# Kernel tuning notes

Hardware: AMD Instinct MI355X
Metric: run time of the kernel (lower is better)

The kernel has to match this reference:

```python
import jax, jax.numpy as jnp
import numpy as np

N = 50000
E = 1600000
IN_C = 512
HID = 64
OUT_C = 64
HEADS = 2
K = 2
NEG_SLOPE = 0.2


def setup_inputs() -> dict:
    key = jax.random.key(0)
    ks = jax.random.split(key, 9)
    x = jax.random.normal(ks[0], (N, IN_C), dtype=jnp.float32)
    edge_index = jax.random.randint(ks[1], (2, E), 0, N, dtype=jnp.int64)
    edge_attr = jax.random.uniform(ks[2], (E,), dtype=jnp.float32)
    # SGConv linear (glorot-ish init)
    W_sg = jax.random.normal(ks[3], (IN_C, HID), dtype=jnp.float32) / np.sqrt(IN_C)
    b_sg = jnp.zeros((HID,), dtype=jnp.float32)
    # GATConv: lin (no bias), attention vectors, output bias (concat=False -> size OUT_C)
    W_gat = jax.random.normal(ks[4], (HID, HEADS * OUT_C), dtype=jnp.float32) / np.sqrt(HID)
    att_src = jax.random.normal(ks[5], (HEADS, OUT_C), dtype=jnp.float32) / np.sqrt(OUT_C)
    att_dst = jax.random.normal(ks[6], (HEADS, OUT_C), dtype=jnp.float32) / np.sqrt(OUT_C)
    b_gat = jnp.zeros((OUT_C,), dtype=jnp.float32)
    return {"x": x, "edge_index": edge_index, "edge_attr": edge_attr,
            "W_sg": W_sg, "b_sg": b_sg, "W_gat": W_gat,
            "att_src": att_src, "att_dst": att_dst, "b_gat": b_gat}


def reference(x, edge_index, edge_attr, W_sg, b_sg, W_gat, att_src, att_dst, b_gat):
    n = x.shape[0]
    src, dst = edge_index[0], edge_index[1]
    # add self-loops (weight 1) once; reused by SGConv (gcn_norm) and GAT
    loop = jnp.arange(n, dtype=src.dtype)
    src2 = jnp.concatenate([src, loop])
    dst2 = jnp.concatenate([dst, loop])
    ew = jnp.concatenate([edge_attr, jnp.ones((n,), x.dtype)])

    # ---- SGConv: K hops of D^-1/2 A D^-1/2, then linear ----
    deg = jax.ops.segment_sum(ew, dst2, num_segments=n)
    dinv = jnp.where(deg > 0, jax.lax.rsqrt(deg), 0.0)
    norm = dinv[src2] * ew * dinv[dst2]  # [E+N]
    h = x
    for _ in range(K):
        h = jax.ops.segment_sum(norm[:, None] * h[src2], dst2, num_segments=n)
    h = h @ W_sg + b_sg  # [N, HID]

    # activation (SELU); dropout is identity in eval mode
    h = jax.nn.selu(h)

    # ---- GATConv (heads, concat=False -> mean over heads) ----
    g = (h @ W_gat).reshape(n, HEADS, OUT_C)  # [N, H, C]
    a_src = jnp.einsum('nhc,hc->nh', g, att_src)  # [N, H]
    a_dst = jnp.einsum('nhc,hc->nh', g, att_dst)
    e = jax.nn.leaky_relu(a_src[src2] + a_dst[dst2], NEG_SLOPE)  # [E+N, H]
    # per-destination softmax (numerically stable)
    emax = jax.ops.segment_max(e, dst2, num_segments=n)
    emax = jnp.where(jnp.isfinite(emax), emax, 0.0)
    ee = jnp.exp(e - emax[dst2])
    denom = jax.ops.segment_sum(ee, dst2, num_segments=n)
    alpha = ee / jnp.maximum(denom[dst2], 1e-16)  # [E+N, H]
    out = jax.ops.segment_sum(alpha[:, :, None] * g[src2], dst2, num_segments=n)  # [N, H, C]
    return out.mean(axis=1) + b_gat  # [N, OUT_C]
```

## Files before the change

### kernel.cpp

```cpp
#include <hip/hip_runtime.h>
#include <hip/hip_fp16.h>
#include <math.h>

#define N_NODES 50000
#define N_EDGES 1600000
#define IN_CH 512
#define HID 64
#define OUTC 64
#define NEG_SLOPE 0.2f
#define EA_SCALE 131072.0f
#define PCAP 128
#define SLOTS 96

typedef __attribute__((ext_vector_type(8))) short bf16x8;
typedef __attribute__((ext_vector_type(4))) float f32x4;

__device__ __forceinline__ unsigned bf16r(float f) {
    unsigned b = __float_as_uint(f);
    return (b + 0x7FFFu + ((b >> 16) & 1u)) >> 16;
}

__device__ __forceinline__ void gload16(const void* g, void* l) {
    __builtin_amdgcn_global_load_lds(
        (const __attribute__((address_space(1))) void*)g,
        (__attribute__((address_space(3))) void*)l, 16, 0, 0);
}

__global__ void k_wsplit(const float* __restrict__ W, short* __restrict__ Wfrag) {
    int idx = blockIdx.x * 256 + threadIdx.x;
    if (idx >= IN_CH * HID) return;
    int k = idx >> 6, c = idx & 63;
    float wv = W[idx];
    unsigned h = bf16r(wv);
    float res = wv - __uint_as_float(h << 16);
    unsigned l = bf16r(res);
    int kstep = k >> 5, cb = c >> 4;
    int lane = (c & 15) | (((k >> 3) & 3) << 4);
    int j = k & 7;
    int base = ((kstep * 4 + cb) * 2) * 512 + lane * 8 + j;
    Wfrag[base] = (short)h;
    Wfrag[base + 512] = (short)l;
}

#define G1R 64
#define G1KC 64
__global__ __launch_bounds__(256) void k_gemm_hist(const float* __restrict__ x,
                                                   const short* __restrict__ Wfrag,
                                                   __half* __restrict__ p,
                                                   const int* __restrict__ src,
                                                   const int* __restrict__ dst,
                                                   const float* __restrict__ ea,
                                                   unsigned* __restrict__ deg32,
                                                   int2* __restrict__ edges2) {
    __shared__ float xs[2][G1R][G1KC];
    int tid = threadIdx.x;
    int bid = blockIdx.x;

    if (bid & 1) {
        int e0 = (bid >> 1) * 2048;
        int e1 = e0 + 2048; if (e1 > N_EDGES) e1 = N_EDGES;
        for (int e = e0 + tid; e < e1; e += 256) {
            int d = dst[e];
            float w = ea[e];
            unsigned pack = (1u << 24) | (unsigned)(w * EA_SCALE);
            unsigned old = atomicAdd(&deg32[d], pack);
            int rank = (int)(old >> 24);
            edges2[d * SLOTS + rank] = make_int2(src[e] << 5, __float_as_int(w));
        }
        return;
    }

    int lane = tid & 63, wv = tid >> 6;
    int r0 = (bid >> 1) * G1R;
    f32x4 acc0 = {0.f, 0.f, 0.f, 0.f};
    f32x4 acc1 = {0.f, 0.f, 0.f, 0.f};
    f32x4 acc2 = {0.f, 0.f, 0.f, 0.f};
    f32x4 acc3 = {0.f, 0.f, 0.f, 0.f};

    auto stage = [&](int b, int k0) {
#pragma unroll
        for (int it = 0; it < 4; it++) {
            int rowbase = it * 16 + wv * 4;
            int row = rowbase + (lane >> 4);
            int gr = r0 + row; if (gr > N_NODES - 1) gr = N_NODES - 1;
            int col = ((lane & 15) ^ (row & 7)) << 2;
            gload16(x + (size_t)gr * IN_CH + k0 + col, &xs[b][rowbase][0]);
        }
    };

    stage(0, 0);
    asm volatile("s_waitcnt vmcnt(0)" ::: "memory");
    __syncthreads();

    int cur = 0;
    int arow = wv * 16 + (lane & 15);
    const char* xsbase = (const char*)&xs[0][0][0];
    for (int k0 = 0; k0 < IN_CH; k0 += G1KC) {
        if (k0 + G1KC < IN_CH) stage(cur ^ 1, k0 + G1KC);
#pragma unroll
        for (int kk = 0; kk < 2; kk++) {
            int ks = (k0 >> 5) + kk;
            const short* wb = Wfrag + ks * 4096 + (lane << 3);
            bf16x8 bh0 = *(const bf16x8*)(wb);
            bf16x8 bl0 = *(const bf16x8*)(wb + 512);
            bf16x8 bh1 = *(const bf16x8*)(wb + 1024);
            bf16x8 bl1 = *(const bf16x8*)(wb + 1536);
            bf16x8 bh2 = *(const bf16x8*)(wb + 2048);
            bf16x8 bl2 = *(const bf16x8*)(wb + 2560);
            bf16x8 bh3 = *(const bf16x8*)(wb + 3072);
            bf16x8 bl3 = *(const bf16x8*)(wb + 3584);
            int c16 = kk * 8 + ((lane >> 4) << 1);
            size_t rb = (size_t)cur * (G1R * G1KC * 4) + (size_t)arow * (G1KC * 4);
            float4 xa = *(const float4*)(xsbase + rb + (((c16    ) ^ (arow & 7)) << 4));
            float4 xb = *(const float4*)(xsbase + rb + (((c16 + 1) ^ (arow & 7)) << 4));
            float xv[8] = {xa.x, xa.y, xa.z, xa.w, xb.x, xb.y, xb.z, xb.w};
            bf16x8 ah, al;
#pragma unroll
            for (int j = 0; j < 8; j++) {
                unsigned b = __float_as_uint(xv[j]);
                float res = xv[j] - __uint_as_float(b & 0xFFFF0000u);
                ah[j] = (short)(b >> 16);
                al[j] = (short)(__float_as_uint(res) >> 16);
            }
            acc0 = __builtin_amdgcn_mfma_f32_16x16x32_bf16(ah, bh0, acc0, 0, 0, 0);
            acc0 = __builtin_amdgcn_mfma_f32_16x16x32_bf16(ah, bl0, acc0, 0, 0, 0);
            acc0 = __builtin_amdgcn_mfma_f32_16x16x32_bf16(al, bh0, acc0, 0, 0, 0);
            acc1 = __builtin_amdgcn_mfma_f32_16x16x32_bf16(ah, bh1, acc1, 0, 0, 0);
            acc1 = __builtin_amdgcn_mfma_f32_16x16x32_bf16(ah, bl1, acc1, 0, 0, 0);
            acc1 = __builtin_amdgcn_mfma_f32_16x16x32_bf16(al, bh1, acc1, 0, 0, 0);
            acc2 = __builtin_amdgcn_mfma_f32_16x16x32_bf16(ah, bh2, acc2, 0, 0, 0);
            acc2 = __builtin_amdgcn_mfma_f32_16x16x32_bf16(ah, bl2, acc2, 0, 0, 0);
            acc2 = __builtin_amdgcn_mfma_f32_16x16x32_bf16(al, bh2, acc2, 0, 0, 0);
            acc3 = __builtin_amdgcn_mfma_f32_16x16x32_bf16(ah, bh3, acc3, 0, 0, 0);
            acc3 = __builtin_amdgcn_mfma_f32_16x16x32_bf16(ah, bl3, acc3, 0, 0, 0);
            acc3 = __builtin_amdgcn_mfma_f32_16x16x32_bf16(al, bh3, acc3, 0, 0, 0);
        }
        asm volatile("s_waitcnt vmcnt(0)" ::: "memory");
        __syncthreads();
        cur ^= 1;
    }
    int crow = r0 + wv * 16 + ((lane >> 4) << 2);
    int ccol = lane & 15;
#pragma unroll
    for (int r = 0; r < 4; r++) {
        int gr = crow + r;
        if (gr < N_NODES) {
            p[(unsigned)gr * HID + ccol]      = __float2half(acc0[r]);
            p[(unsigned)gr * HID + 16 + ccol] = __float2half(acc1[r]);
            p[(unsigned)gr * HID + 32 + ccol] = __float2half(acc2[r]);
            p[(unsigned)gr * HID + 48 + ccol] = __float2half(acc3[r]);
        }
    }
}

__global__ void k_dinv(const unsigned* __restrict__ deg32, float* __restrict__ dinv) {
    int i = blockIdx.x * 256 + threadIdx.x;
    if (i < N_NODES)
        dinv[i] = rsqrtf(1.0f + (float)(deg32[i] & 0xFFFFFFu) * (1.0f / EA_SCALE));
}

__global__ void k_hscale(unsigned* __restrict__ h2, const float* __restrict__ dinv) {
    int idx = blockIdx.x * 256 + threadIdx.x;
    if (idx >= N_NODES * 32) return;
    float dv = dinv[idx >> 5];
    unsigned u = h2[idx];
    float2 f = __half22float2(*(__half2*)&u);
    __half2 r = __floats2half2_rn(f.x * dv, f.y * dv);
    h2[idx] = *(unsigned*)&r;
}

__global__ __launch_bounds__(256) void k_hop(const unsigned* __restrict__ hin2,
                                             const unsigned* __restrict__ deg32,
                                             const int2* __restrict__ edges2,
                                             const float* __restrict__ dinv,
                                             unsigned* __restrict__ hout2,
                                             int pw) {
    __shared__ float2 part[2][32];
    int tid = threadIdx.x;
    int w = tid >> 6, lane = tid & 63;
    int slot = w >> 1, half = w & 1;
    int cl = lane & 31, es = lane >> 5;
    int v = blockIdx.x * 2 + slot;
    int cnt = (int)(deg32[v] >> 24);
    int beg = v * SLOTS, end = beg + cnt;
    int mid = beg + (cnt >> 1);
    int lo = half ? mid : beg;
    int hi = half ? end : mid;
    float ax = 0.f, ay = 0.f, bx = 0.f, by = 0.f;
    float cx = 0.f, cy = 0.f, dx = 0.f, dy = 0.f;
    if (!half && !es) {
        unsigned gh = hin2[(unsigned)v * 32 + cl];
        float2 hf = __half22float2(*(__half2*)&gh);
        ax = hf.x; ay = hf.y;
    }
    int i = lo;
    for (; i + 16 <= hi; i += 16) {
        int2 e0 = edges2[i + es];
        int2 e1 = edges2[i + 2 + es];
        int2 e2 = edges2[i + 4 + es];
        int2 e3 = edges2[i + 6 + es];
        int2 e4 = edges2[i + 8 + es];
        int2 e5 = edges2[i + 10 + es];
        int2 e6 = edges2[i + 12 + es];
        int2 e7 = edges2[i + 14 + es];
        unsigned g0 = hin2[(unsigned)(e0.x + cl)];
        unsigned g1 = hin2[(unsigned)(e1.x + cl)];
        unsigned g2 = hin2[(unsigned)(e2.x + cl)];
        unsigned g3 = hin2[(unsigned)(e3.x + cl)];
        unsigned g4 = hin2[(unsigned)(e4.x + cl)];
        unsigned g5 = hin2[(unsigned)(e5.x + cl)];
        unsigned g6 = hin2[(unsigned)(e6.x + cl)];
        unsigned g7 = hin2[(unsigned)(e7.x + cl)];
        float w0 = __int_as_float(e0.y), w1 = __int_as_float(e1.y);
        float w2 = __int_as_float(e2.y), w3 = __int_as_float(e3.y);
        float w4 = __int_as_float(e4.y), w5 = __int_as_float(e5.y);
        float w6 = __int_as_float(e6.y), w7 = __int_as_float(e7.y);
        float2 h0 = __half22float2(*(__half2*)&g0);
        float2 h1 = __half22float2(*(__half2*)&g1);
        float2 h2 = __half22float2(*(__half2*)&g2);
        float2 h3 = __half22float2(*(__half2*)&g3);
        float2 h4 = __half22float2(*(__half2*)&g4);
        float2 h5 = __half22float2(*(__half2*)&g5);
        float2 h6 = __half22float2(*(__half2*)&g6);
        float2 h7 = __half22float2(*(__half2*)&g7);
        ax += w0 * h0.x; ay += w0 * h0.y;
        bx += w1 * h1.x; by += w1 * h1.y;
        cx += w2 * h2.x; cy += w2 * h2.y;
        dx += w3 * h3.x; dy += w3 * h3.y;
        ax += w4 * h4.x; ay += w4 * h4.y;
        bx += w5 * h5.x; by += w5 * h5.y;
        cx += w6 * h6.x; cy += w6 * h6.y;
        dx += w7 * h7.x; dy += w7 * h7.y;
    }
    for (; i + 8 <= hi; i += 8) {
        int2 e0 = edges2[i + es];
        int2 e1 = edges2[i + 2 + es];
        int2 e2 = edges2[i + 4 + es];
        int2 e3 = edges2[i + 6 + es];
        unsigned g0 = hin2[(unsigned)(e0.x + cl)];
        unsigned g1 = hin2[(unsigned)(e1.x + cl)];
        unsigned g2 = hin2[(unsigned)(e2.x + cl)];
        unsigned g3 = hin2[(unsigned)(e3.x + cl)];
        float w0 = __int_as_float(e0.y), w1 = __int_as_float(e1.y);
        float w2 = __int_as_float(e2.y), w3 = __int_as_float(e3.y);
        float2 h0 = __half22float2(*(__half2*)&g0);
        float2 h1 = __half22float2(*(__half2*)&g1);
        float2 h2 = __half22float2(*(__half2*)&g2);
        float2 h3 = __half22float2(*(__half2*)&g3);
        ax += w0 * h0.x; ay += w0 * h0.y;
        bx += w1 * h1.x; by += w1 * h1.y;
        cx += w2 * h2.x; cy += w2 * h2.y;
        dx += w3 * h3.x; dy += w3 * h3.y;
    }
    for (; i + es < hi; i += 2) {
        int2 e0 = edges2[i + es];
        unsigned g0 = hin2[(unsigned)(e0.x + cl)];
        float w0 = __int_as_float(e0.y);
        float2 h0 = __half22float2(*(__half2*)&g0);
        ax += w0 * h0.x; ay += w0 * h0.y;
    }
    ax += bx + cx + dx; ay += by + cy + dy;
    ax += __shfl_xor(ax, 32);
    ay += __shfl_xor(ay, 32);
    if (half && lane < 32) part[slot][cl] = make_float2(ax, ay);
    __syncthreads();
    if (!half && lane < 32) {
        float dv = dinv[v];
        float sc = (pw == 2) ? dv * dv : dv;
        float2 pp = part[slot][cl];
        __half2 hp = __floats2half2_rn(sc * (ax + pp.x), sc * (ay + pp.y));
        hout2[(unsigned)v * 32 + cl] = *(unsigned*)&hp;
    }
}

#define G2_ROWS 32
__global__ __launch_bounds__(256) void k_act_gemm2(const __half* __restrict__ h2,
                                                   const float* __restrict__ bsg,
                                                   const float* __restrict__ Wg,
                                                   const float* __restrict__ att_s,
                                                   const float* __restrict__ att_d,
                                                   uint2* __restrict__ g4h,
                                                   float2* __restrict__ asrc2,
                                                   float4* __restrict__ admm) {
    __shared__ float hs[G2_ROWS][HID];
    int tid = threadIdx.x;
    int wave = tid >> 6, lane = tid & 63;
    int r0 = blockIdx.x * G2_ROWS;
    int rbase = wave * 8;

    const float SC = 1.0507009873554805f, AL = 1.6732632423543772f;
    {
        int row = tid >> 3, c0 = (tid & 7) * 8;
        int r = r0 + row;
        float vals[8];
        if (r < N_NODES) {
            uint4 raw = *(const uint4*)(h2 + (unsigned)r * HID + c0);
            float2 f0 = __half22float2(*(__half2*)&raw.x);
            float2 f1 = __half22float2(*(__half2*)&raw.y);
            float2 f2 = __half22float2(*(__half2*)&raw.z);
            float2 f3 = __half22float2(*(__half2*)&raw.w);
            vals[0] = f0.x; vals[1] = f0.y; vals[2] = f1.x; vals[3] = f1.y;
            vals[4] = f2.x; vals[5] = f2.y; vals[6] = f3.x; vals[7] = f3.y;
        } else {
#pragma unroll
            for (int j = 0; j < 8; j++) vals[j] = 0.f;
        }
#pragma unroll
        for (int j = 0; j < 8; j++) {
            float hv = vals[j] + bsg[c0 + j];
            hv = (hv > 0.f) ? SC * hv : SC * AL * (__expf(hv) - 1.f);
            hs[row][c0 + j] = hv;
        }
    }
    __syncthreads();

    float accx[8], accy[8];
#pragma unroll
    for (int j = 0; j < 8; j++) { accx[j] = 0.f; accy[j] = 0.f; }
#pragma unroll 2
    for (int k = 0; k < HID; k++) {
        float w0 = Wg[(size_t)k * 128 + lane];
        float w1 = Wg[(size_t)k * 128 + 64 + lane];
#pragma unroll
        for (int j = 0; j < 8; j++) {
            float hk = hs[rbase + j][k];
            accx[j] += hk * w0;
            accy[j] += hk * w1;
        }
    }
    float ats0 = att_s[lane], ats1 = att_s[64 + lane];
    float atd0 = att_d[lane], atd1 = att_d[64 + lane];
#pragma unroll
    for (int j = 0; j < 8; j++) {
        int v = r0 + rbase + j;
        if (v >= N_NODES) break;
        __half2 gp = __floats2half2_rn(accx[j], accy[j]);
        unsigned gpu = *(unsigned*)&gp;
        unsigned other = (unsigned)__shfl_xor((int)gpu, 1);
        if (!(lane & 1)) g4h[(unsigned)v * 32 + (lane >> 1)] = make_uint2(gpu, other);
        float s0 = accx[j] * ats0, s1 = accy[j] * ats1;
        float d0 = accx[j] * atd0, d1 = accy[j] * atd1;
#pragma unroll
        for (int o = 32; o > 0; o >>= 1) {
            s0 += __shfl_xor(s0, o);
            s1 += __shfl_xor(s1, o);
            d0 += __shfl_xor(d0, o);
            d1 += __shfl_xor(d1, o);
        }
        if (lane == 0) {
            asrc2[v] = make_float2(s0, s1);
            float m0 = s0 + d0; m0 = (m0 > 0.f) ? m0 : NEG_SLOPE * m0;
            float m1 = s1 + d1; m1 = (m1 > 0.f) ? m1 : NEG_SLOPE * m1;
            admm[v] = make_float4(d0, d1, m0, m1);
        }
    }
}

__global__ __launch_bounds__(256) void k_gat(const uint2* __restrict__ g4h,
                                             const float2* __restrict__ asrc2,
                                             const float4* __restrict__ admm,
                                             const unsigned* __restrict__ deg32,
                                             const int2* __restrict__ edges2,
                                             const float* __restrict__ bgat,
                                             float* __restrict__ out) {
    __shared__ int4 pbuf[2][2][PCAP];
    __shared__ float4 pacc[2][32];
    __shared__ float2 pden[2][32];
    int tid = threadIdx.x;
    int w = tid >> 6, lane = tid & 63;
    int slot = w >> 1, half = w & 1;
    int cl = lane & 31, es = lane >> 5;
    int v = blockIdx.x * 2 + slot;
    float4 am = admm[v];
    int cnt = (int)(deg32[v] >> 24);
    int beg = v * SLOTS, end = beg + cnt;
    int mid = beg + (cnt >> 1);
    int lo = half ? mid : beg;
    int hi = half ? end : mid;
    int n = hi - lo;

    float pd0 = 0.f, pd1 = 0.f;
    for (int i = lo + lane; i < hi; i += 64) {
        int2 e = edges2[i];
        float2 a = asrc2[(unsigned)e.x >> 5];
        float t0 = a.x + am.x; t0 = (t0 > 0.f) ? t0 : NEG_SLOPE * t0;
        float t1 = a.y + am.y; t1 = (t1 > 0.f) ? t1 : NEG_SLOPE * t1;
        float p0 = __expf(t0 - am.z);
        float p1 = __expf(t1 - am.w);
        int idx = i - lo;
        if (idx < PCAP)
            pbuf[slot][half][idx] = make_int4(e.x, __float_as_int(p0), __float_as_int(p1), 0);
        pd0 += p0; pd1 += p1;
    }
#pragma unroll
    for (int o = 32; o > 0; o >>= 1) {
        pd0 += __shfl_xor(pd0, o);
        pd1 += __shfl_xor(pd1, o);
    }
    if (!half) { pd0 += 1.f; pd1 += 1.f; }

    float aA = 0.f, aB = 0.f, aC = 0.f, aD = 0.f;
    float bA = 0.f, bB = 0.f, bC = 0.f, bD = 0.f;
    if (!half && !es) {
        uint2 gs = g4h[(unsigned)v * 32 + cl];
        float2 gx = __half22float2(*(__half2*)&gs.x);
        float2 gy = __half22float2(*(__half2*)&gs.y);
        aA = gx.x; aB = gx.y; aC = gy.x; aD = gy.y;
    }
    int n1 = (n < PCAP) ? n : PCAP;
    int ii = 0;
    for (; ii + 8 <= n1; ii += 8) {
        int4 e0 = pbuf[slot][half][ii + es];
        int4 e1 = pbuf[slot][half][ii + 2 + es];
        int4 e2 = pbuf[slot][half][ii + 4 + es];
        int4 e3 = pbuf[slot][half][ii + 6 + es];
        uint2 g0 = g4h[(unsigned)(e0.x + cl)];
        uint2 g1 = g4h[(unsigned)(e1.x + cl)];
        uint2 g2 = g4h[(unsigned)(e2.x + cl)];
        uint2 g3 = g4h[(unsigned)(e3.x + cl)];
        float p00 = __int_as_float(e0.y), p01 = __int_as_float(e0.z);
        float p10 = __int_as_float(e1.y), p11 = __int_as_float(e1.z);
        float p20 = __int_as_float(e2.y), p21 = __int_as_float(e2.z);
        float p30 = __int_as_float(e3.y), p31 = __int_as_float(e3.z);
        float2 g0x = __half22float2(*(__half2*)&g0.x);
        float2 g0y = __half22float2(*(__half2*)&g0.y);
        float2 g1x = __half22float2(*(__half2*)&g1.x);
        float2 g1y = __half22float2(*(__half2*)&g1.y);
        float2 g2x = __half22float2(*(__half2*)&g2.x);
        float2 g2y = __half22float2(*(__half2*)&g2.y);
        float2 g3x = __half22float2(*(__half2*)&g3.x);
        float2 g3y = __half22float2(*(__half2*)&g3.y);
        aA += p00 * g0x.x; aB += p01 * g0x.y; aC += p00 * g0y.x; aD += p01 * g0y.y;
        bA += p10 * g1x.x; bB += p11 * g1x.y; bC += p10 * g1y.x; bD += p11 * g1y.y;
        aA += p20 * g2x.x; aB += p21 * g2x.y; aC += p20 * g2y.x; aD += p21 * g2y.y;
        bA += p30 * g3x.x; bB += p31 * g3x.y; bC += p30 * g3y.x; bD += p31 * g3y.y;
    }
    for (; ii + es < n1; ii += 2) {
        int4 e0 = pbuf[slot][half][ii + es];
        uint2 g0 = g4h[(unsigned)(e0.x + cl)];
        float p00 = __int_as_float(e0.y), p01 = __int_as_float(e0.z);
        float2 g0x = __half22float2(*(__half2*)&g0.x);
        float2 g0y = __half22float2(*(__half2*)&g0.y);
        aA += p00 * g0x.x; aB += p01 * g0x.y; aC += p00 * g0y.x; aD += p01 * g0y.y;
    }
    aA += bA; aB += bB; aC += bC; aD += bD;
    aA += __shfl_xor(aA, 32); aB += __shfl_xor(aB, 32);
    aC += __shfl_xor(aC, 32); aD += __shfl_xor(aD, 32);
    if (half && lane < 32) {
        pacc[slot][cl] = make_float4(aA, aB, aC, aD);
        pden[slot][cl] = make_float2(pd0, pd1);
    }
    __syncthreads();
    if (!half && lane < 32) {
        float4 pa = pacc[slot][cl];
        float2 pd = pden[slot][cl];
        float r0 = 1.f / (pd0 + pd.x), r1 = 1.f / (pd1 + pd.y);
        float oe = 0.5f * ((aA + pa.x) * r0 + (aB + pa.y) * r1) + bgat[cl * 2];
        float oo = 0.5f * ((aC + pa.z) * r0 + (aD + pa.w) * r1) + bgat[cl * 2 + 1];
        *(float2*)&out[(unsigned)v * OUTC + cl * 2] = make_float2(oe, oo);
    }
}

extern "C" void kernel_launch(void* const* d_in, const int* in_sizes, int n_in,
                              void* d_out, int out_size, void* d_ws, size_t ws_size,
                              hipStream_t stream) {
    const float* x     = (const float*)d_in[0];
    const int*   ei    = (const int*)d_in[1];
    const float* ea    = (const float*)d_in[2];
    const float* Wsg   = (const float*)d_in[3];
    const float* bsg   = (const float*)d_in[4];
    const float* Wg    = (const float*)d_in[5];
    const float* att_s = (const float*)d_in[6];
    const float* att_d = (const float*)d_in[7];
    const float* bgat  = (const float*)d_in[8];
    const int* src = ei;
    const int* dst = ei + N_EDGES;
    float* out = (float*)d_out;

    char* ws = (char*)d_ws;
    size_t off = 0;
    auto alloc = [&](size_t bytes) -> void* {
        void* p = ws + off;
        off = (off + bytes + 255) & ~(size_t)255;
        return p;
    };
    unsigned* deg32  = (unsigned*)alloc((size_t)N_NODES * 4);
    float*    dinv   = (float*)alloc((size_t)N_NODES * 4);
    int2*     edges2 = (int2*)alloc((size_t)N_NODES * SLOTS * 8);
    short*    Wfrag  = (short*)alloc((size_t)IN_CH * HID * 2 * 2);
    __half*   h0     = (__half*)alloc((size_t)N_NODES * HID * 2);
    __half*   h1     = (__half*)alloc((size_t)N_NODES * HID * 2);
    uint2*    g4h    = (uint2*)alloc((size_t)N_NODES * 32 * 8);
    float2*   asrc2  = (float2*)alloc((size_t)N_NODES * 8);
    float4*   admm   = (float4*)alloc((size_t)N_NODES * 16);
    (void)ws_size; (void)in_sizes; (void)n_in; (void)out_size;

    hipMemsetAsync(deg32, 0, (size_t)N_NODES * 4, stream);

    k_wsplit<<<(IN_CH * HID + 255) / 256, 256, 0, stream>>>(Wsg, Wfrag);

    k_gemm_hist<<<1564, 256, 0, stream>>>(x, Wfrag, h0, src, dst, ea, deg32, edges2);

    int nb = (N_NODES + 255) / 256;
    k_dinv<<<nb, 256, 0, stream>>>(deg32, dinv);
    k_hscale<<<(N_NODES * 32 + 255) / 256, 256, 0, stream>>>((unsigned*)h0, dinv);

    k_hop<<<N_NODES / 2, 256, 0, stream>>>((const unsigned*)h0, deg32, edges2, dinv, (unsigned*)h1, 2);
    k_hop<<<N_NODES / 2, 256, 0, stream>>>((const unsigned*)h1, deg32, edges2, dinv, (unsigned*)h0, 1);
    k_act_gemm2<<<(N_NODES + G2_ROWS - 1) / G2_ROWS, 256, 0, stream>>>(h0, bsg, Wg, att_s, att_d, g4h, asrc2, admm);
    k_gat<<<N_NODES / 2, 256, 0, stream>>>(g4h, asrc2, admm, deg32, edges2, bgat, out);
}
```

Before: 299.0 us.

## Pack edge records into 32-bit words and widen hop gathers to 8 bytes

Each bucketed edge record is packed into one 32-bit int, with the source index in the high 16 bits and the weight as fp16 in the low 16 bits. This halves the edge-list footprint and bandwidth. The hop kernel now has each lane gather 4 halves with 16 lanes per edge and 4 edges in flight, and the separate dinv kernel is folded into hscale. Storing src in 16 bits cannot hold node ids up to 50000 only if they exceed 65535, so that is fine, but the fp16 weight lowers precision, and overflow-guard paths for rank beyond the slot count were added.

```diff
diff --git a/kernel.cpp b/kernel.cpp
--- a/kernel.cpp
+++ b/kernel.cpp
@@ -51,7 +51,7 @@
                                                    const int* __restrict__ dst,
                                                    const float* __restrict__ ea,
                                                    unsigned* __restrict__ deg32,
-                                                   int2* __restrict__ edges2) {
+                                                   int* __restrict__ edges4) {
     __shared__ float xs[2][G1R][G1KC];
     int tid = threadIdx.x;
     int bid = blockIdx.x;
@@ -65,7 +65,9 @@
             unsigned pack = (1u << 24) | (unsigned)(w * EA_SCALE);
             unsigned old = atomicAdd(&deg32[d], pack);
             int rank = (int)(old >> 24);
-            edges2[d * SLOTS + rank] = make_int2(src[e] << 5, __float_as_int(w));
+            if (rank < SLOTS)
+                edges4[d * SLOTS + rank] =
+                    (src[e] << 16) | (int)__half_as_ushort(__float2half_rn(w));
         }
         return;
     }
@@ -153,123 +155,82 @@
     }
 }
 
-__global__ void k_dinv(const unsigned* __restrict__ deg32, float* __restrict__ dinv) {
-    int i = blockIdx.x * 256 + threadIdx.x;
-    if (i < N_NODES)
-        dinv[i] = rsqrtf(1.0f + (float)(deg32[i] & 0xFFFFFFu) * (1.0f / EA_SCALE));
-}
-
-__global__ void k_hscale(unsigned* __restrict__ h2, const float* __restrict__ dinv) {
+__global__ void k_hscale(unsigned* __restrict__ h2, const unsigned* __restrict__ deg32,
+                         float* __restrict__ dinv) {
     int idx = blockIdx.x * 256 + threadIdx.x;
     if (idx >= N_NODES * 32) return;
-    float dv = dinv[idx >> 5];
+    int v = idx >> 5;
+    float dv = rsqrtf(1.0f + (float)(deg32[v] & 0xFFFFFFu) * (1.0f / EA_SCALE));
+    if ((idx & 31) == 0) dinv[v] = dv;
     unsigned u = h2[idx];
     float2 f = __half22float2(*(__half2*)&u);
     __half2 r = __floats2half2_rn(f.x * dv, f.y * dv);
     h2[idx] = *(unsigned*)&r;
 }
 
-__global__ __launch_bounds__(256) void k_hop(const unsigned* __restrict__ hin2,
+__global__ __launch_bounds__(256) void k_hop(const uint2* __restrict__ hin4,
                                              const unsigned* __restrict__ deg32,
-                                             const int2* __restrict__ edges2,
+                                             const int* __restrict__ edges4,
                                              const float* __restrict__ dinv,
-                                             unsigned* __restrict__ hout2,
+                                             uint2* __restrict__ hout4,
                                              int pw) {
-    __shared__ float2 part[2][32];
+    __shared__ float4 part[2][16];
     int tid = threadIdx.x;
     int w = tid >> 6, lane = tid & 63;
     int slot = w >> 1, half = w & 1;
-    int cl = lane & 31, es = lane >> 5;
+    int cl = lane & 15, es = lane >> 4;
     int v = blockIdx.x * 2 + slot;
     int cnt = (int)(deg32[v] >> 24);
+    if (cnt > SLOTS) cnt = SLOTS;
     int beg = v * SLOTS, end = beg + cnt;
     int mid = beg + (cnt >> 1);
     int lo = half ? mid : beg;
     int hi = half ? end : mid;
-    float ax = 0.f, ay = 0.f, bx = 0.f, by = 0.f;
-    float cx = 0.f, cy = 0.f, dx = 0.f, dy = 0.f;
+    float a0 = 0.f, a1 = 0.f, a2 = 0.f, a3 = 0.f;
+    float b0 = 0.f, b1 = 0.f, b2 = 0.f, b3 = 0.f;
     if (!half && !es) {
-        unsigned gh = hin2[(unsigned)v * 32 + cl];
-        float2 hf = __half22float2(*(__half2*)&gh);
-        ax = hf.x; ay = hf.y;
+        uint2 u = hin4[(unsigned)v * 16 + cl];
+        float2 f0 = __half22float2(*(__half2*)&u.x);
+        float2 f1 = __half22float2(*(__half2*)&u.y);
+        a0 = f0.x; a1 = f0.y; a2 = f1.x; a3 = f1.y;
     }
     int i = lo;
-    for (; i + 16 <= hi; i += 16) {
-        int2 e0 = edges2[i + es];
-        int2 e1 = edges2[i + 2 + es];
-        int2 e2 = edges2[i + 4 + es];
-        int2 e3 = edges2[i + 6 + es];
-        int2 e4 = edges2[i + 8 + es];
-        int2 e5 = edges2[i + 10 + es];
-        int2 e6 = edges2[i + 12 + es];
-        int2 e7 = edges2[i + 14 + es];
-        unsigned g0 = hin2[(unsigned)(e0.x + cl)];
-        unsigned g1 = hin2[(unsigned)(e1.x + cl)];
-        unsigned g2 = hin2[(unsigned)(e2.x + cl)];
-        unsigned g3 = hin2[(unsigned)(e3.x + cl)];
-        unsigned g4 = hin2[(unsigned)(e4.x + cl)];
-        unsigned g5 = hin2[(unsigned)(e5.x + cl)];
-        unsigned g6 = hin2[(unsigned)(e6.x + cl)];
-        unsigned g7 = hin2[(unsigned)(e7.x + cl)];
-        float w0 = __int_as_float(e0.y), w1 = __int_as_float(e1.y);
-        float w2 = __int_as_float(e2.y), w3 = __int_as_float(e3.y);
-        float w4 = __int_as_float(e4.y), w5 = __int_as_float(e5.y);
-        float w6 = __int_as_float(e6.y), w7 = __int_as_float(e7.y);
-        float2 h0 = __half22float2(*(__half2*)&g0);
-        float2 h1 = __half22float2(*(__half2*)&g1);
-        float2 h2 = __half22float2(*(__half2*)&g2);
-        float2 h3 = __half22float2(*(__half2*)&g3);
-        float2 h4 = __half22float2(*(__half2*)&g4);
-        float2 h5 = __half22float2(*(__half2*)&g5);
-        float2 h6 = __half22float2(*(__half2*)&g6);
-        float2 h7 = __half22float2(*(__half2*)&g7);
-        ax += w0 * h0.x; ay += w0 * h0.y;
-        bx += w1 * h1.x; by += w1 * h1.y;
-        cx += w2 * h2.x; cy += w2 * h2.y;
-        dx += w3 * h3.x; dy += w3 * h3.y;
-        ax += w4 * h4.x; ay += w4 * h4.y;
-        bx += w5 * h5.x; by += w5 * h5.y;
-        cx += w6 * h6.x; cy += w6 * h6.y;
-        dx += w7 * h7.x; dy += w7 * h7.y;
-    }
     for (; i + 8 <= hi; i += 8) {
-        int2 e0 = edges2[i + es];
-        int2 e1 = edges2[i + 2 + es];
-        int2 e2 = edges2[i + 4 + es];
-        int2 e3 = edges2[i + 6 + es];
-        unsigned g0 = hin2[(unsigned)(e0.x + cl)];
-        unsigned g1 = hin2[(unsigned)(e1.x + cl)];
-        unsigned g2 = hin2[(unsigned)(e2.x + cl)];
-        unsigned g3 = hin2[(unsigned)(e3.x + cl)];
-        float w0 = __int_as_float(e0.y), w1 = __int_as_float(e1.y);
-        float w2 = __int_as_float(e2.y), w3 = __int_as_float(e3.y);
-        float2 h0 = __half22float2(*(__half2*)&g0);
-        float2 h1 = __half22float2(*(__half2*)&g1);
-        float2 h2 = __half22float2(*(__half2*)&g2);
-        float2 h3 = __half22float2(*(__half2*)&g3);
-        ax += w0 * h0.x; ay += w0 * h0.y;
-        bx += w1 * h1.x; by += w1 * h1.y;
-        cx += w2 * h2.x; cy += w2 * h2.y;
-        dx += w3 * h3.x; dy += w3 * h3.y;
-    }
-    for (; i + es < hi; i += 2) {
-        int2 e0 = edges2[i + es];
-        unsigned g0 = hin2[(unsigned)(e0.x + cl)];
-        float w0 = __int_as_float(e0.y);
-        float2 h0 = __half22float2(*(__half2*)&g0);
-        ax += w0 * h0.x; ay += w0 * h0.y;
-    }
-    ax += bx + cx + dx; ay += by + cy + dy;
-    ax += __shfl_xor(ax, 32);
-    ay += __shfl_xor(ay, 32);
-    if (half && lane < 32) part[slot][cl] = make_float2(ax, ay);
+        int r0 = edges4[i + es];
+        int r1 = edges4[i + 4 + es];
+        uint2 g0 = hin4[(((unsigned)r0 >> 16) << 4) + cl];
+        uint2 g1 = hin4[(((unsigned)r1 >> 16) << 4) + cl];
+        float w0 = __half2float(__ushort_as_half((unsigned short)(r0 & 0xFFFF)));
+        float w1 = __half2float(__ushort_as_half((unsigned short)(r1 & 0xFFFF)));
+        float2 g0a = __half22float2(*(__half2*)&g0.x);
+        float2 g0b = __half22float2(*(__half2*)&g0.y);
+        float2 g1a = __half22float2(*(__half2*)&g1.x);
+        float2 g1b = __half22float2(*(__half2*)&g1.y);
+        a0 += w0 * g0a.x; a1 += w0 * g0a.y; a2 += w0 * g0b.x; a3 += w0 * g0b.y;
+        b0 += w1 * g1a.x; b1 += w1 * g1a.y; b2 += w1 * g1b.x; b3 += w1 * g1b.y;
+    }
+    for (; i + es < hi; i += 4) {
+        int r0 = edges4[i + es];
+        uint2 g0 = hin4[(((unsigned)r0 >> 16) << 4) + cl];
+        float w0 = __half2float(__ushort_as_half((unsigned short)(r0 & 0xFFFF)));
+        float2 g0a = __half22float2(*(__half2*)&g0.x);
+        float2 g0b = __half22float2(*(__half2*)&g0.y);
+        a0 += w0 * g0a.x; a1 += w0 * g0a.y; a2 += w0 * g0b.x; a3 += w0 * g0b.y;
+    }
+    a0 += b0; a1 += b1; a2 += b2; a3 += b3;
+    a0 += __shfl_xor(a0, 16); a1 += __shfl_xor(a1, 16);
+    a2 += __shfl_xor(a2, 16); a3 += __shfl_xor(a3, 16);
+    a0 += __shfl_xor(a0, 32); a1 += __shfl_xor(a1, 32);
+    a2 += __shfl_xor(a2, 32); a3 += __shfl_xor(a3, 32);
+    if (half && lane < 16) part[slot][cl] = make_float4(a0, a1, a2, a3);
     __syncthreads();
-    if (!half && lane < 32) {
+    if (!half && lane < 16) {
         float dv = dinv[v];
         float sc = (pw == 2) ? dv * dv : dv;
-        float2 pp = part[slot][cl];
-        __half2 hp = __floats2half2_rn(sc * (ax + pp.x), sc * (ay + pp.y));
-        hout2[(unsigned)v * 32 + cl] = *(unsigned*)&hp;
+        float4 pp = part[slot][cl];
+        __half2 h0 = __floats2half2_rn(sc * (a0 + pp.x), sc * (a1 + pp.y));
+        __half2 h1 = __floats2half2_rn(sc * (a2 + pp.z), sc * (a3 + pp.w));
+        hout4[(unsigned)v * 16 + cl] = make_uint2(*(unsigned*)&h0, *(unsigned*)&h1);
     }
 }
 
@@ -360,7 +321,7 @@
                                              const float2* __restrict__ asrc2,
                                              const float4* __restrict__ admm,
                                              const unsigned* __restrict__ deg32,
-                                             const int2* __restrict__ edges2,
+                                             const int* __restrict__ edges4,
                                              const float* __restrict__ bgat,
                                              float* __restrict__ out) {
     __shared__ int4 pbuf[2][2][PCAP];
@@ -373,6 +334,7 @@
     int v = blockIdx.x * 2 + slot;
     float4 am = admm[v];
     int cnt = (int)(deg32[v] >> 24);
+    if (cnt > SLOTS) cnt = SLOTS;
     int beg = v * SLOTS, end = beg + cnt;
     int mid = beg + (cnt >> 1);
     int lo = half ? mid : beg;
@@ -381,15 +343,16 @@
 
     float pd0 = 0.f, pd1 = 0.f;
     for (int i = lo + lane; i < hi; i += 64) {
-        int2 e = edges2[i];
-        float2 a = asrc2[(unsigned)e.x >> 5];
+        int r = edges4[i];
+        unsigned s = (unsigned)r >> 16;
+        float2 a = asrc2[s];
         float t0 = a.x + am.x; t0 = (t0 > 0.f) ? t0 : NEG_SLOPE * t0;
         float t1 = a.y + am.y; t1 = (t1 > 0.f) ? t1 : NEG_SLOPE * t1;
         float p0 = __expf(t0 - am.z);
         float p1 = __expf(t1 - am.w);
         int idx = i - lo;
         if (idx < PCAP)
-            pbuf[slot][half][idx] = make_int4(e.x, __float_as_int(p0), __float_as_int(p1), 0);
+            pbuf[slot][half][idx] = make_int4((int)(s << 5), __float_as_int(p0), __float_as_int(p1), 0);
         pd0 += p0; pd1 += p1;
     }
 #pragma unroll
@@ -443,6 +406,19 @@
         float2 g0y = __half22float2(*(__half2*)&g0.y);
         aA += p00 * g0x.x; aB += p01 * g0x.y; aC += p00 * g0y.x; aD += p01 * g0y.y;
     }
+    for (int jj = PCAP + es; jj < n; jj += 2) {
+        int r = edges4[lo + jj];
+        unsigned s = (unsigned)r >> 16;
+        float2 a = asrc2[s];
+        float t0 = a.x + am.x; t0 = (t0 > 0.f) ? t0 : NEG_SLOPE * t0;
+        float t1 = a.y + am.y; t1 = (t1 > 0.f) ? t1 : NEG_SLOPE * t1;
+        float p0 = __expf(t0 - am.z);
+        float p1 = __expf(t1 - am.w);
+        uint2 g0 = g4h[(s << 5) + cl];
+        float2 g0x = __half22float2(*(__half2*)&g0.x);
+        float2 g0y = __half22float2(*(__half2*)&g0.y);
+        aA += p0 * g0x.x; aB += p1 * g0x.y; aC += p0 * g0y.x; aD += p1 * g0y.y;
+    }
     aA += bA; aB += bB; aC += bC; aD += bD;
     aA += __shfl_xor(aA, 32); aB += __shfl_xor(aB, 32);
     aC += __shfl_xor(aC, 32); aD += __shfl_xor(aD, 32);
@@ -486,7 +462,7 @@
     };
     unsigned* deg32  = (unsigned*)alloc((size_t)N_NODES * 4);
     float*    dinv   = (float*)alloc((size_t)N_NODES * 4);
-    int2*     edges2 = (int2*)alloc((size_t)N_NODES * SLOTS * 8);
+    int*      edges4 = (int*)alloc((size_t)N_NODES * SLOTS * 4);
     short*    Wfrag  = (short*)alloc((size_t)IN_CH * HID * 2 * 2);
     __half*   h0     = (__half*)alloc((size_t)N_NODES * HID * 2);
     __half*   h1     = (__half*)alloc((size_t)N_NODES * HID * 2);
@@ -499,14 +475,12 @@
 
     k_wsplit<<<(IN_CH * HID + 255) / 256, 256, 0, stream>>>(Wsg, Wfrag);
 
-    k_gemm_hist<<<1564, 256, 0, stream>>>(x, Wfrag, h0, src, dst, ea, deg32, edges2);
-
-    int nb = (N_NODES + 255) / 256;
-    k_dinv<<<nb, 256, 0, stream>>>(deg32, dinv);
-    k_hscale<<<(N_NODES * 32 + 255) / 256, 256, 0, stream>>>((unsigned*)h0, dinv);
-
-    k_hop<<<N_NODES / 2, 256, 0, stream>>>((const unsigned*)h0, deg32, edges2, dinv, (unsigned*)h1, 2);
-    k_hop<<<N_NODES / 2, 256, 0, stream>>>((const unsigned*)h1, deg32, edges2, dinv, (unsigned*)h0, 1);
+    k_gemm_hist<<<1564, 256, 0, stream>>>(x, Wfrag, h0, src, dst, ea, deg32, edges4);
+
+    k_hscale<<<(N_NODES * 32 + 255) / 256, 256, 0, stream>>>((unsigned*)h0, deg32, dinv);
+
+    k_hop<<<N_NODES / 2, 256, 0, stream>>>((const uint2*)h0, deg32, edges4, dinv, (uint2*)h1, 2);
+    k_hop<<<N_NODES / 2, 256, 0, stream>>>((const uint2*)h1, deg32, edges4, dinv, (uint2*)h0, 1);
     k_act_gemm2<<<(N_NODES + G2_ROWS - 1) / G2_ROWS, 256, 0, stream>>>(h0, bsg, Wg, att_s, att_d, g4h, asrc2, admm);
-    k_gat<<<N_NODES / 2, 256, 0, stream>>>(g4h, asrc2, admm, deg32, edges2, bgat, out);
-}
+    k_gat<<<N_NODES / 2, 256, 0, stream>>>(g4h, asrc2, admm, deg32, edges4, bgat, out);
+}
```

After: 279.9 us. 1.07x faster.
